# Performance work log

Measured on AMD Instinct MI355X. Metric: run time of the kernel, lower is better.

Reference implementation:

```python
import jax, jax.numpy as jnp
import numpy as np

B = 131072
# join branch layer dims: 203 -> 175 -> 150 -> 128 -> 80 -> 48
DIMS = [203, 175, 150, 128, 80, 48]

def setup_inputs() -> dict:
    key = jax.random.key(0)
    ks = jax.random.split(key, 11)
    inp = {"x": jax.random.normal(ks[0], (B, DIMS[0]), dtype=jnp.float32)}
    for i in range(5):
        fan_in, fan_out = DIMS[i], DIMS[i + 1]
        bound = 1.0 / np.sqrt(fan_in)
        inp[f"W{i+1}"] = jax.random.uniform(ks[1 + 2 * i], (fan_out, fan_in), minval=-bound, maxval=bound, dtype=jnp.float32)
        inp[f"b{i+1}"] = jax.random.uniform(ks[2 + 2 * i], (fan_out,), minval=-bound, maxval=bound, dtype=jnp.float32)
    return inp

def reference(x, W1, b1, W2, b2, W3, b3, W4, b4, W5, b5):
    # join branch of NodeEmbedding, dropout in eval mode (identity).
    h = jnp.tanh(x @ W1.T + b1)      # [B,175]
    h = jnp.tanh(h @ W2.T + b2)      # [B,150]
    h = jnp.tanh(h @ W3.T + b3)      # [B,128]
    h = jnp.tanh(h @ W4.T + b4)      # [B,80]
    return h @ W5.T + b5             # [B,48], no activation on last layer
```

## Files before the change

### kernel.cpp

```cpp
#include <hip/hip_runtime.h>


typedef short short8 __attribute__((ext_vector_type(8)));
typedef float f32x16 __attribute__((ext_vector_type(16)));
typedef unsigned int uint;
typedef unsigned short ushort;

#define SROW 180
#define XSTR 20

__device__ __forceinline__ ushort f2bf(float f) {
    uint u = __float_as_uint(f);
    u += 0x7FFFu + ((u >> 16) & 1u);
    return (ushort)(u >> 16);
}
__device__ __forceinline__ float bf2f(ushort h) { return __uint_as_float(((uint)h) << 16); }
__device__ __forceinline__ float fast_tanh(float x) {
    float e = __expf(2.0f * x);
    return 1.0f - 2.0f / (e + 1.0f);
}
__device__ __forceinline__ uint rbf(float v) {
    uint u = __float_as_uint(v);
    return u + 0x7FFFu + ((u >> 16) & 1u);
}

union U4S8 { uint4 u; short8 s; };

__global__ void prep_weights(const float* __restrict__ W1, const float* __restrict__ W2,
                             const float* __restrict__ W3, const float* __restrict__ W4,
                             const float* __restrict__ W5, char* __restrict__ ws)
{
    const int b = blockIdx.x, l = threadIdx.x;
    int layer, local;
    if      (b <  78) { layer = 0; local = b; }
    else if (b < 133) { layer = 1; local = b - 78; }
    else if (b < 173) { layer = 2; local = b - 133; }
    else if (b < 197) { layer = 3; local = b - 173; }
    else              { layer = 4; local = b - 197; }
    const int NTa[5]  = {6, 5, 4, 3, 2};
    const int FINa[5] = {203, 175, 150, 128, 80};
    const int FOa[5]  = {175, 150, 128, 80, 48};
    const float* Wp = (layer == 0) ? W1 : (layer == 1) ? W2 : (layer == 2) ? W3
                    : (layer == 3) ? W4 : W5;
    const int nt = NTa[layer], fin = FINa[layer], fout = FOa[layer];
    const int c = local / nt, t = local % nt;
    const int n  = t * 32 + (l & 31);
    const int kb = c * 16 + (l >> 5) * 8;
    uint hw[4], lw[4];
#pragma unroll
    for (int j = 0; j < 8; ++j) {
        int k = kb + j;
        float v = (n < fout && k < fin) ? Wp[(size_t)n * fin + k] : 0.0f;
        ushort hh = f2bf(v);
        ushort ll = f2bf(v - bf2f(hh));
        if (j & 1) { hw[j >> 1] |= ((uint)hh) << 16; lw[j >> 1] |= ((uint)ll) << 16; }
        else       { hw[j >> 1]  = hh;               lw[j >> 1]  = ll; }
    }
    char* dst = ws + (size_t)b * 2048 + l * 16;
    *(uint4*)dst          = make_uint4(hw[0], hw[1], hw[2], hw[3]);
    *(uint4*)(dst + 1024) = make_uint4(lw[0], lw[1], lw[2], lw[3]);
}

template<int MT, int NT, int FOUT, int PADN, bool ACT, bool LAST>
__device__ __forceinline__ void d_phase(f32x16* acc, uint* oP, float* outg,
                                        int row0, int rg, int ns, int lx, int lh, int tid)
{
#pragma unroll
    for (int m = 0; m < MT; ++m) {
        int t = ns + 2 * m;
        if (t < NT) {
#pragma unroll
            for (int r = 0; r < 16; ++r) {
                float vv = acc[m][r];
                if (ACT) vv = fast_tanh(vv);
                int rowl = rg * 32 + (r & 3) + 8 * (r >> 2) + 4 * lh;
                int col  = t * 32 + lx;
                if (LAST) {
                    if (col < 48) outg[(size_t)(row0 + rowl) * 48 + col] = vv;
                } else if (col < FOUT) {
                    uint r1  = rbf(vv);
                    uint hib = r1 & 0xFFFF0000u;
                    float lo = vv - __uint_as_float(hib);
                    uint r2  = rbf(lo);
                    oP[rowl * SROW + col] = hib | (r2 >> 16);
                }
            }
        }
    }
    if (!LAST) {
        if (PADN > 0) {
            for (int idx = tid; idx < 64 * PADN; idx += 256) {
                int row = idx / PADN, p = idx % PADN;
                oP[row * SROW + FOUT + p] = 0u;
            }
        }
        __syncthreads();
    }
}

template<int KC, int NT, int FOUT, int PADN, bool ACT, bool LAST>
__device__ __forceinline__ void run_layer(const char* __restrict__ wsL,
    const float* __restrict__ bias, const uint* aP, uint* oP, float* outg,
    int row0, int l, int rg, int ns, int lx, int lh, int tid)
{
    constexpr int MT = (NT + 1) / 2;
    f32x16 acc[MT];
#pragma unroll
    for (int m = 0; m < MT; ++m) {
        int t = ns + 2 * m;
        float bv = 0.0f;
        if (t < NT) { int n = t * 32 + lx; bv = (n < FOUT) ? bias[n] : 0.0f; }
#pragma unroll
        for (int r = 0; r < 16; ++r) acc[m][r] = bv;
    }

#pragma unroll
    for (int c = 0; c < KC; ++c) {
        U4S8 bh[MT], bl[MT];
#pragma unroll
        for (int m = 0; m < MT; ++m) {
            int t = ns + 2 * m;
            if (t < NT) {
                const uint4* w = (const uint4*)wsL + (size_t)((c * NT + t) * 2) * 64 + l;
                bh[m].u = w[0];
                bl[m].u = w[64];
            }
        }
        const uint* ap = aP + (rg * 32 + lx) * SROW + c * 16 + lh * 8;
        uint4 d0 = *(const uint4*)ap;
        uint4 d1 = *(const uint4*)(ap + 4);
        uint dd[8] = {d0.x, d0.y, d0.z, d0.w, d1.x, d1.y, d1.z, d1.w};
        U4S8 ah, al;
        uint* aHu = (uint*)&ah; uint* aLu = (uint*)&al;
#pragma unroll
        for (int j = 0; j < 4; ++j) {
            aHu[j] = (dd[2*j] >> 16)     | (dd[2*j + 1] & 0xFFFF0000u);
            aLu[j] = (dd[2*j] & 0xFFFFu) | (dd[2*j + 1] << 16);
        }
#pragma unroll
        for (int m = 0; m < MT; ++m) {
            int t = ns + 2 * m;
            if (t < NT) {
                acc[m] = __builtin_amdgcn_mfma_f32_32x32x16_bf16(ah.s, bh[m].s, acc[m], 0, 0, 0);
                acc[m] = __builtin_amdgcn_mfma_f32_32x32x16_bf16(al.s, bh[m].s, acc[m], 0, 0, 0);
                acc[m] = __builtin_amdgcn_mfma_f32_32x32x16_bf16(ah.s, bl[m].s, acc[m], 0, 0, 0);
            }
        }
    }
    if (!LAST) __syncthreads();
    d_phase<MT, NT, FOUT, PADN, ACT, LAST>(acc, oP, outg, row0, rg, ns, lx, lh, tid);
}

__device__ __forceinline__ void run_first(const float* __restrict__ x,
    const char* __restrict__ wsL, const float* __restrict__ bias,
    uint* oP, float* xst, int row0, int l, int rg, int ns, int lx, int lh, int tid)
{
    constexpr int KC = 13, NT = 6, MT = 3;
    f32x16 acc[MT];
#pragma unroll
    for (int m = 0; m < MT; ++m) {
        int n = (ns + 2 * m) * 32 + lx;
        float bv = (n < 175) ? bias[n] : 0.0f;
#pragma unroll
        for (int r = 0; r < 16; ++r) acc[m][r] = bv;
    }

#pragma unroll
    for (int i = 0; i < 4; ++i) {
        int e = i * 256 + tid, row = e >> 4, kk = e & 15;
        xst[row * XSTR + kk] = x[(size_t)(row0 + row) * 203 + kk];
    }
    __syncthreads();

#pragma unroll
    for (int c = 0; c < KC; ++c) {
        U4S8 bh[MT], bl[MT];
#pragma unroll
        for (int m = 0; m < MT; ++m) {
            const uint4* w = (const uint4*)wsL + (size_t)((c * 6 + ns + 2 * m) * 2) * 64 + l;
            bh[m].u = w[0];
            bl[m].u = w[64];
        }
        float pre[4];
        if (c < 12) {
#pragma unroll
            for (int i = 0; i < 4; ++i) {
                int e = i * 256 + tid, row = e >> 4, kk = e & 15, k = (c + 1) * 16 + kk;
                pre[i] = (k < 203) ? x[(size_t)(row0 + row) * 203 + k] : 0.0f;
            }
        }
        const float* apf = xst + (rg * 32 + lx) * XSTR + lh * 8;
        float4 v0 = *(const float4*)apf;
        float4 v1 = *(const float4*)(apf + 4);
        float vv[8] = {v0.x, v0.y, v0.z, v0.w, v1.x, v1.y, v1.z, v1.w};
        uint rh[8], rl[8];
#pragma unroll
        for (int j = 0; j < 8; ++j) {
            rh[j] = rbf(vv[j]);
            float lo = vv[j] - __uint_as_float(rh[j] & 0xFFFF0000u);
            rl[j] = rbf(lo);
        }
        U4S8 ah, al;
        uint* aHu = (uint*)&ah; uint* aLu = (uint*)&al;
#pragma unroll
        for (int j = 0; j < 4; ++j) {
            aHu[j] = (rh[2*j] >> 16) | (rh[2*j + 1] & 0xFFFF0000u);
            aLu[j] = (rl[2*j] >> 16) | (rl[2*j + 1] & 0xFFFF0000u);
        }
#pragma unroll
        for (int m = 0; m < MT; ++m) {
            acc[m] = __builtin_amdgcn_mfma_f32_32x32x16_bf16(ah.s, bh[m].s, acc[m], 0, 0, 0);
            acc[m] = __builtin_amdgcn_mfma_f32_32x32x16_bf16(al.s, bh[m].s, acc[m], 0, 0, 0);
            acc[m] = __builtin_amdgcn_mfma_f32_32x32x16_bf16(ah.s, bl[m].s, acc[m], 0, 0, 0);
        }
        if (c < 12) {
            __syncthreads();
#pragma unroll
            for (int i = 0; i < 4; ++i) {
                int e = i * 256 + tid, row = e >> 4, kk = e & 15;
                xst[row * XSTR + kk] = pre[i];
            }
            __syncthreads();
        }
    }
    d_phase<MT, NT, 175, 1, true, false>(acc, oP, nullptr, row0, rg, ns, lx, lh, tid);
}

__global__ __launch_bounds__(256, 3)
void mlp_mfma(const float* __restrict__ x,
              const float* __restrict__ b1, const float* __restrict__ b2,
              const float* __restrict__ b3, const float* __restrict__ b4,
              const float* __restrict__ b5,
              const char* __restrict__ ws, float* __restrict__ out)
{
    __shared__ __align__(16) uint  actP[64 * SROW];
    __shared__ __align__(16) float xst[64 * XSTR];

    const int tid = threadIdx.x;
    const int l = tid & 63, w = tid >> 6;
    const int rg = w >> 1, ns = w & 1;
    const int lx = l & 31, lh = l >> 5;
    const int row0 = blockIdx.x * 64;

    run_first(x, ws, b1, actP, xst, row0, l, rg, ns, lx, lh, tid);
    run_layer<11, 5, 150, 10, true,  false>(ws +  78 * 2048, b2, actP, actP, nullptr, row0, l, rg, ns, lx, lh, tid);
    run_layer<10, 4, 128,  0, true,  false>(ws + 133 * 2048, b3, actP, actP, nullptr, row0, l, rg, ns, lx, lh, tid);
    run_layer< 8, 3,  80,  0, true,  false>(ws + 173 * 2048, b4, actP, actP, nullptr, row0, l, rg, ns, lx, lh, tid);
    run_layer< 5, 2,  48,  0, false, true >(ws + 197 * 2048, b5, actP, actP, out,     row0, l, rg, ns, lx, lh, tid);
}

extern "C" void kernel_launch(void* const* d_in, const int* in_sizes, int n_in,
                              void* d_out, int out_size, void* d_ws, size_t ws_size,
                              hipStream_t stream) {
    (void)in_sizes; (void)n_in; (void)ws_size; (void)out_size;
    const float* x  = (const float*)d_in[0];
    const float* W1 = (const float*)d_in[1];
    const float* b1 = (const float*)d_in[2];
    const float* W2 = (const float*)d_in[3];
    const float* b2 = (const float*)d_in[4];
    const float* W3 = (const float*)d_in[5];
    const float* b3 = (const float*)d_in[6];
    const float* W4 = (const float*)d_in[7];
    const float* b4 = (const float*)d_in[8];
    const float* W5 = (const float*)d_in[9];
    const float* b5 = (const float*)d_in[10];
    float* out = (float*)d_out;
    char* ws = (char*)d_ws;

    hipLaunchKernelGGL(prep_weights, dim3(207), dim3(64), 0, stream,
                       W1, W2, W3, W4, W5, ws);
    hipLaunchKernelGGL(mlp_mfma, dim3(131072 / 64), dim3(256), 0, stream,
                       x, b1, b2, b3, b4, b5, ws, out);
}
```

Measured before the change: 298.8 us.

## Fuse weight prep into MLP kernel, store activations as single bf16

Merges the weight-preparation kernel into the main kernel, so that every block redundantly converts all weights into the workspace before processing two 64-row tiles on a persistent grid of 1024 blocks. Hidden activations are now stored as a single bf16 instead of a split hi/lo pair, which cuts the MFMAs in layers 2-5 from three to two per tile and halves activation LDS traffic. It also uses packed bf16 conversion intrinsics and raises the occupancy hint to 4 blocks per CU. The risks are reduced precision from the single-bf16 activations and a race, since blocks write the shared workspace concurrently and there is no grid-wide barrier before other blocks read it, plus the redundant prep work done in every block.

```diff
diff --git a/kernel.cpp b/kernel.cpp
--- a/kernel.cpp
+++ b/kernel.cpp
@@ -1,4 +1,5 @@
 #include <hip/hip_runtime.h>
+#include <hip/hip_bf16.h>
 
 
 typedef short short8 __attribute__((ext_vector_type(8)));
@@ -6,31 +7,32 @@
 typedef unsigned int uint;
 typedef unsigned short ushort;
 
-#define SROW 180
+#define SROWU 184
 #define XSTR 20
-
+#define GRID 1024
+
+union BF2U { __hip_bfloat162 b; uint u; };
+
+__device__ __forceinline__ uint pk_bf16(float a, float b) {
+    BF2U t; t.b = __float22bfloat162_rn(make_float2(a, b)); return t.u;
+}
 __device__ __forceinline__ ushort f2bf(float f) {
     uint u = __float_as_uint(f);
     u += 0x7FFFu + ((u >> 16) & 1u);
     return (ushort)(u >> 16);
 }
-__device__ __forceinline__ float bf2f(ushort h) { return __uint_as_float(((uint)h) << 16); }
 __device__ __forceinline__ float fast_tanh(float x) {
     float e = __expf(2.0f * x);
     return 1.0f - 2.0f / (e + 1.0f);
 }
-__device__ __forceinline__ uint rbf(float v) {
-    uint u = __float_as_uint(v);
-    return u + 0x7FFFu + ((u >> 16) & 1u);
-}
 
 union U4S8 { uint4 u; short8 s; };
 
-__global__ void prep_weights(const float* __restrict__ W1, const float* __restrict__ W2,
-                             const float* __restrict__ W3, const float* __restrict__ W4,
-                             const float* __restrict__ W5, char* __restrict__ ws)
-{
-    const int b = blockIdx.x, l = threadIdx.x;
+__device__ __forceinline__ void prep_pair(int b, int l,
+    const float* __restrict__ W1, const float* __restrict__ W2,
+    const float* __restrict__ W3, const float* __restrict__ W4,
+    const float* __restrict__ W5, char* __restrict__ ws)
+{
     int layer, local;
     if      (b <  78) { layer = 0; local = b; }
     else if (b < 133) { layer = 1; local = b - 78; }
@@ -46,23 +48,28 @@
     const int c = local / nt, t = local % nt;
     const int n  = t * 32 + (l & 31);
     const int kb = c * 16 + (l >> 5) * 8;
-    uint hw[4], lw[4];
+    float v[8];
 #pragma unroll
     for (int j = 0; j < 8; ++j) {
         int k = kb + j;
-        float v = (n < fout && k < fin) ? Wp[(size_t)n * fin + k] : 0.0f;
-        ushort hh = f2bf(v);
-        ushort ll = f2bf(v - bf2f(hh));
-        if (j & 1) { hw[j >> 1] |= ((uint)hh) << 16; lw[j >> 1] |= ((uint)ll) << 16; }
-        else       { hw[j >> 1]  = hh;               lw[j >> 1]  = ll; }
-    }
-    char* dst = ws + (size_t)b * 2048 + l * 16;
-    *(uint4*)dst          = make_uint4(hw[0], hw[1], hw[2], hw[3]);
-    *(uint4*)(dst + 1024) = make_uint4(lw[0], lw[1], lw[2], lw[3]);
+        v[j] = (n < fout && k < fin) ? Wp[(size_t)n * fin + k] : 0.0f;
+    }
+    uint hw[4], lw[4];
+#pragma unroll
+    for (int j = 0; j < 4; ++j) {
+        uint hp = pk_bf16(v[2*j], v[2*j+1]);
+        float h0 = __uint_as_float(hp << 16);
+        float h1 = __uint_as_float(hp & 0xFFFF0000u);
+        hw[j] = hp;
+        lw[j] = pk_bf16(v[2*j] - h0, v[2*j+1] - h1);
+    }
+    uint4* dst = (uint4*)(ws + (size_t)b * 2048) + l;
+    dst[0]  = make_uint4(hw[0], hw[1], hw[2], hw[3]);
+    dst[64] = make_uint4(lw[0], lw[1], lw[2], lw[3]);
 }
 
 template<int MT, int NT, int FOUT, int PADN, bool ACT, bool LAST>
-__device__ __forceinline__ void d_phase(f32x16* acc, uint* oP, float* outg,
+__device__ __forceinline__ void d_phase(f32x16* acc, ushort* oP, float* outg,
                                         int row0, int rg, int ns, int lx, int lh, int tid)
 {
 #pragma unroll
@@ -78,11 +85,7 @@
                 if (LAST) {
                     if (col < 48) outg[(size_t)(row0 + rowl) * 48 + col] = vv;
                 } else if (col < FOUT) {
-                    uint r1  = rbf(vv);
-                    uint hib = r1 & 0xFFFF0000u;
-                    float lo = vv - __uint_as_float(hib);
-                    uint r2  = rbf(lo);
-                    oP[rowl * SROW + col] = hib | (r2 >> 16);
+                    oP[rowl * SROWU + col] = f2bf(vv);
                 }
             }
         }
@@ -91,7 +94,7 @@
         if (PADN > 0) {
             for (int idx = tid; idx < 64 * PADN; idx += 256) {
                 int row = idx / PADN, p = idx % PADN;
-                oP[row * SROW + FOUT + p] = 0u;
+                oP[row * SROWU + FOUT + p] = 0;
             }
         }
         __syncthreads();
@@ -100,7 +103,7 @@
 
 template<int KC, int NT, int FOUT, int PADN, bool ACT, bool LAST>
 __device__ __forceinline__ void run_layer(const char* __restrict__ wsL,
-    const float* __restrict__ bias, const uint* aP, uint* oP, float* outg,
+    const float* __restrict__ bias, const ushort* aP, ushort* oP, float* outg,
     int row0, int l, int rg, int ns, int lx, int lh, int tid)
 {
     constexpr int MT = (NT + 1) / 2;
@@ -126,24 +129,14 @@
                 bl[m].u = w[64];
             }
         }
-        const uint* ap = aP + (rg * 32 + lx) * SROW + c * 16 + lh * 8;
-        uint4 d0 = *(const uint4*)ap;
-        uint4 d1 = *(const uint4*)(ap + 4);
-        uint dd[8] = {d0.x, d0.y, d0.z, d0.w, d1.x, d1.y, d1.z, d1.w};
-        U4S8 ah, al;
-        uint* aHu = (uint*)&ah; uint* aLu = (uint*)&al;
-#pragma unroll
-        for (int j = 0; j < 4; ++j) {
-            aHu[j] = (dd[2*j] >> 16)     | (dd[2*j + 1] & 0xFFFF0000u);
-            aLu[j] = (dd[2*j] & 0xFFFFu) | (dd[2*j + 1] << 16);
-        }
+        U4S8 a;
+        a.u = *(const uint4*)(aP + (rg * 32 + lx) * SROWU + c * 16 + lh * 8);
 #pragma unroll
         for (int m = 0; m < MT; ++m) {
             int t = ns + 2 * m;
             if (t < NT) {
-                acc[m] = __builtin_amdgcn_mfma_f32_32x32x16_bf16(ah.s, bh[m].s, acc[m], 0, 0, 0);
-                acc[m] = __builtin_amdgcn_mfma_f32_32x32x16_bf16(al.s, bh[m].s, acc[m], 0, 0, 0);
-                acc[m] = __builtin_amdgcn_mfma_f32_32x32x16_bf16(ah.s, bl[m].s, acc[m], 0, 0, 0);
+                acc[m] = __builtin_amdgcn_mfma_f32_32x32x16_bf16(a.s, bh[m].s, acc[m], 0, 0, 0);
+                acc[m] = __builtin_amdgcn_mfma_f32_32x32x16_bf16(a.s, bl[m].s, acc[m], 0, 0, 0);
             }
         }
     }
@@ -153,9 +146,9 @@
 
 __device__ __forceinline__ void run_first(const float* __restrict__ x,
     const char* __restrict__ wsL, const float* __restrict__ bias,
-    uint* oP, float* xst, int row0, int l, int rg, int ns, int lx, int lh, int tid)
-{
-    constexpr int KC = 13, NT = 6, MT = 3;
+    ushort* oP, float* xst, int row0, int l, int rg, int ns, int lx, int lh, int tid)
+{
+    constexpr int KC = 13, MT = 3;
     f32x16 acc[MT];
 #pragma unroll
     for (int m = 0; m < MT; ++m) {
@@ -193,19 +186,15 @@
         float4 v0 = *(const float4*)apf;
         float4 v1 = *(const float4*)(apf + 4);
         float vv[8] = {v0.x, v0.y, v0.z, v0.w, v1.x, v1.y, v1.z, v1.w};
-        uint rh[8], rl[8];
-#pragma unroll
-        for (int j = 0; j < 8; ++j) {
-            rh[j] = rbf(vv[j]);
-            float lo = vv[j] - __uint_as_float(rh[j] & 0xFFFF0000u);
-            rl[j] = rbf(lo);
-        }
         U4S8 ah, al;
         uint* aHu = (uint*)&ah; uint* aLu = (uint*)&al;
 #pragma unroll
         for (int j = 0; j < 4; ++j) {
-            aHu[j] = (rh[2*j] >> 16) | (rh[2*j + 1] & 0xFFFF0000u);
-            aLu[j] = (rl[2*j] >> 16) | (rl[2*j + 1] & 0xFFFF0000u);
+            uint hp = pk_bf16(vv[2*j], vv[2*j+1]);
+            float h0 = __uint_as_float(hp << 16);
+            float h1 = __uint_as_float(hp & 0xFFFF0000u);
+            aHu[j] = hp;
+            aLu[j] = pk_bf16(vv[2*j] - h0, vv[2*j+1] - h1);
         }
 #pragma unroll
         for (int m = 0; m < MT; ++m) {
@@ -223,30 +212,42 @@
             __syncthreads();
         }
     }
-    d_phase<MT, NT, 175, 1, true, false>(acc, oP, nullptr, row0, rg, ns, lx, lh, tid);
-}
-
-__global__ __launch_bounds__(256, 3)
-void mlp_mfma(const float* __restrict__ x,
-              const float* __restrict__ b1, const float* __restrict__ b2,
-              const float* __restrict__ b3, const float* __restrict__ b4,
-              const float* __restrict__ b5,
-              const char* __restrict__ ws, float* __restrict__ out)
-{
-    __shared__ __align__(16) uint  actP[64 * SROW];
-    __shared__ __align__(16) float xst[64 * XSTR];
+    d_phase<MT, 6, 175, 1, true, false>(acc, oP, nullptr, row0, rg, ns, lx, lh, tid);
+}
+
+__global__ __launch_bounds__(256, 4)
+void mlp_fused(const float* __restrict__ x,
+               const float* __restrict__ W1, const float* __restrict__ b1,
+               const float* __restrict__ W2, const float* __restrict__ b2,
+               const float* __restrict__ W3, const float* __restrict__ b3,
+               const float* __restrict__ W4, const float* __restrict__ b4,
+               const float* __restrict__ W5, const float* __restrict__ b5,
+               char* __restrict__ ws, float* __restrict__ out)
+{
+    __shared__ __align__(16) ushort actP[64 * SROWU];
+    __shared__ __align__(16) float  xst[64 * XSTR];
 
     const int tid = threadIdx.x;
+
+#pragma unroll 1
+    for (int task = tid; task < 207 * 64; task += 256)
+        prep_pair(task >> 6, task & 63, W1, W2, W3, W4, W5, ws);
+    __threadfence();
+    __syncthreads();
+
     const int l = tid & 63, w = tid >> 6;
     const int rg = w >> 1, ns = w & 1;
     const int lx = l & 31, lh = l >> 5;
-    const int row0 = blockIdx.x * 64;
-
-    run_first(x, ws, b1, actP, xst, row0, l, rg, ns, lx, lh, tid);
-    run_layer<11, 5, 150, 10, true,  false>(ws +  78 * 2048, b2, actP, actP, nullptr, row0, l, rg, ns, lx, lh, tid);
-    run_layer<10, 4, 128,  0, true,  false>(ws + 133 * 2048, b3, actP, actP, nullptr, row0, l, rg, ns, lx, lh, tid);
-    run_layer< 8, 3,  80,  0, true,  false>(ws + 173 * 2048, b4, actP, actP, nullptr, row0, l, rg, ns, lx, lh, tid);
-    run_layer< 5, 2,  48,  0, false, true >(ws + 197 * 2048, b5, actP, actP, out,     row0, l, rg, ns, lx, lh, tid);
+
+#pragma unroll 1
+    for (int it = 0; it < 2; ++it) {
+        const int row0 = (blockIdx.x + it * GRID) * 64;
+        run_first(x, ws, b1, actP, xst, row0, l, rg, ns, lx, lh, tid);
+        run_layer<11, 5, 150, 10, true,  false>(ws +  78 * 2048, b2, actP, actP, nullptr, row0, l, rg, ns, lx, lh, tid);
+        run_layer<10, 4, 128,  0, true,  false>(ws + 133 * 2048, b3, actP, actP, nullptr, row0, l, rg, ns, lx, lh, tid);
+        run_layer< 8, 3,  80,  0, true,  false>(ws + 173 * 2048, b4, actP, actP, nullptr, row0, l, rg, ns, lx, lh, tid);
+        run_layer< 5, 2,  48,  0, false, true >(ws + 197 * 2048, b5, actP, actP, out,     row0, l, rg, ns, lx, lh, tid);
+    }
 }
 
 extern "C" void kernel_launch(void* const* d_in, const int* in_sizes, int n_in,
@@ -267,8 +268,6 @@
     float* out = (float*)d_out;
     char* ws = (char*)d_ws;
 
-    hipLaunchKernelGGL(prep_weights, dim3(207), dim3(64), 0, stream,
-                       W1, W2, W3, W4, W5, ws);
-    hipLaunchKernelGGL(mlp_mfma, dim3(131072 / 64), dim3(256), 0, stream,
-                       x, b1, b2, b3, b4, b5, ws, out);
-}
+    hipLaunchKernelGGL(mlp_fused, dim3(GRID), dim3(256), 0, stream,
+                       x, W1, b1, W2, b2, W3, b3, W4, b4, W5, b5, ws, out);
+}
```

Result: slower. 975.5 us (+226.5%).
